# Performance work log

Measured on AMD Instinct MI355X. Metric: run time of the kernel, lower is better.

Reference implementation:

```python
import jax, jax.numpy as jnp
import numpy as np

N = 100000
IN_C, HID_C, OUT_C = 128, 128, 64
E = 1600000


def setup_inputs() -> dict:
    key = jax.random.key(0)
    ks = jax.random.split(key, 8)
    x = jax.random.normal(ks[0], (N, IN_C), dtype=jnp.float32)
    edge_index = jax.random.randint(ks[1], (2, E), 0, N, dtype=jnp.int64)
    def glorot(k, fan_in, fan_out):
        lim = np.sqrt(6.0 / (fan_in + fan_out)).astype(np.float32)
        return jax.random.uniform(k, (fan_in, fan_out), jnp.float32, -lim, lim)
    return {
        "x": x,
        "edge_index": edge_index,
        "W1l": glorot(ks[2], IN_C, HID_C),   # lin_l: aggregated neighbors
        "W1r": glorot(ks[3], IN_C, HID_C),   # lin_r: root/self
        "b1": jnp.zeros((HID_C,), jnp.float32),
        "W2l": glorot(ks[4], HID_C, OUT_C),
        "W2r": glorot(ks[5], HID_C, OUT_C),
        "b2": jnp.zeros((OUT_C,), jnp.float32),
    }


def _sage_conv(x, src, dst, Wl, Wr, b):
    # mean aggregation over incoming edges: gather source feats, segment-sum at dst
    msg_sum = jax.ops.segment_sum(x[src], dst, num_segments=N)          # [N, C_in]
    deg = jax.ops.segment_sum(jnp.ones((src.shape[0],), x.dtype), dst,
                              num_segments=N)                           # [N]
    mean = msg_sum / jnp.clip(deg, 1.0, None)[:, None]
    return mean @ Wl + x @ Wr + b


def reference(x, edge_index, W1l, W1r, b1, W2l, W2r, b2):
    src, dst = edge_index[0], edge_index[1]
    h = jax.nn.relu(_sage_conv(x, src, dst, W1l, W1r, b1))
    out = _sage_conv(h, src, dst, W2l, W2r, b2)
    return out
```

## Files before the change

### kernel.cpp

```cpp
#include <hip/hip_runtime.h>
#include <type_traits>


constexpr int K = 128;
constexpr int EB = 2048;
constexpr int CAP = 8192;

typedef __bf16 bf16x2 __attribute__((ext_vector_type(2)));
typedef __bf16 bf16x4 __attribute__((ext_vector_type(4)));
typedef __bf16 bf16x8 __attribute__((ext_vector_type(8)));
typedef float f32x4 __attribute__((ext_vector_type(4)));
typedef float f32x2 __attribute__((ext_vector_type(2)));


__device__ __forceinline__ unsigned char to_fp8(float v) {
#if __has_builtin(__builtin_amdgcn_cvt_pk_fp8_f32)
  int p = __builtin_amdgcn_cvt_pk_fp8_f32(v, v, 0, false);
  return (unsigned char)(p & 0xff);
#else
  unsigned u = __builtin_bit_cast(unsigned, v);
  unsigned s = (u >> 24) & 0x80u;
  float a = fabsf(v);
  if (a > 448.f) a = 448.f;
  unsigned bits;
  if (a < 0.015625f) {
    bits = (unsigned)(a * 512.f + 0.5f);
  } else {
    unsigned b = __builtin_bit_cast(unsigned, a);
    b += ((b >> 20) & 1) + 0x0007FFFF;
    unsigned e = (b >> 23) - 120;
    bits = (e << 3) | ((b >> 20) & 7);
    if (bits > 0x7E) bits = 0x7E;
  }
  return (unsigned char)(s | bits);
#endif
}

__device__ __forceinline__ f32x2 from_fp8x2(unsigned short u) {
#if __has_builtin(__builtin_amdgcn_cvt_pk_f32_fp8)
  return __builtin_amdgcn_cvt_pk_f32_fp8((int)u, false);
#else
  f32x2 r;
  unsigned b0 = u & 0xff, b1 = (u >> 8) & 0xff;
  unsigned e0 = (b0 >> 3) & 15, m0 = b0 & 7;
  unsigned e1 = (b1 >> 3) & 15, m1 = b1 & 7;
  float v0 = e0 ? __builtin_bit_cast(float, ((e0 + 120) << 23) | (m0 << 20))
              : (float)m0 * 0.001953125f;
  float v1 = e1 ? __builtin_bit_cast(float, ((e1 + 120) << 23) | (m1 << 20))
              : (float)m1 * 0.001953125f;
  r[0] = (b0 & 0x80) ? -v0 : v0;
  r[1] = (b1 & 0x80) ? -v1 : v1;
  return r;
#endif
}

__device__ __forceinline__ f32x2 fp8x2_lo(unsigned v) {
#if __has_builtin(__builtin_amdgcn_cvt_pk_f32_fp8)
  return __builtin_amdgcn_cvt_pk_f32_fp8((int)v, false);
#else
  return from_fp8x2((unsigned short)(v & 0xffffu));
#endif
}

__device__ __forceinline__ f32x2 fp8x2_hi(unsigned v) {
#if __has_builtin(__builtin_amdgcn_cvt_pk_f32_fp8)
  return __builtin_amdgcn_cvt_pk_f32_fp8((int)v, true);
#else
  return from_fp8x2((unsigned short)(v >> 16));
#endif
}


__global__ __launch_bounds__(256) void k_scatter(const int* __restrict__ src,
                                                 const int* __restrict__ dst,
                                                 int* __restrict__ bucketCount,
                                                 unsigned* __restrict__ recs,
                                                 int E, int n, int nB) {
  extern __shared__ int cur[];
  for (int i = threadIdx.x; i < nB; i += 256) cur[i] = 0;
  __syncthreads();
  int base = blockIdx.x * EB, end = min(base + EB, E);
  for (int e = base + threadIdx.x; e < end; e += 256) {
    int d = dst[e];
    if ((unsigned)d < (unsigned)n) atomicAdd(&cur[d >> 8], 1);
  }
  __syncthreads();
  for (int i = threadIdx.x; i < nB; i += 256) {
    int c = cur[i];
    cur[i] = c ? atomicAdd(&bucketCount[i], c) : 0;
  }
  __syncthreads();
  for (int e = base + threadIdx.x; e < end; e += 256) {
    int d = dst[e];
    if ((unsigned)d < (unsigned)n) {
      int s = min(max(src[e], 0), n - 1);
      int b = d >> 8;
      int pos = min(atomicAdd(&cur[b], 1), CAP - 1);
      recs[(long)b * CAP + pos] = ((unsigned)s << 8) | (unsigned)(d & 255);
    }
  }
}

__global__ __launch_bounds__(256) void k_bfill(const unsigned* __restrict__ recs,
                                               const int* __restrict__ bucketCount,
                                               int* __restrict__ rowptr,
                                               int* __restrict__ col, int n) {
  __shared__ int degl[256];
  __shared__ int incl[256];
  __shared__ int red[256];
  int b = blockIdx.x, t = threadIdx.x;

  int partial = 0;
  for (int i = t; i < b; i += 256) partial += bucketCount[i];
  red[t] = partial;
  __syncthreads();
  for (int off = 128; off > 0; off >>= 1) {
    if (t < off) red[t] += red[t + off];
    __syncthreads();
  }
  int rbeg = red[0];
  int cnt = bucketCount[b];
  const unsigned* rbase = recs + (long)b * CAP;
  __syncthreads();

  degl[t] = 0;
  __syncthreads();
  for (int i = t; i < cnt; i += 256)
    atomicAdd(&degl[rbase[i] & 255], 1);
  __syncthreads();
  incl[t] = degl[t];
  __syncthreads();
  for (int off = 1; off < 256; off <<= 1) {
    int v = (t >= off) ? incl[t - off] : 0;
    __syncthreads();
    incl[t] += v;
    __syncthreads();
  }
  int excl = incl[t] - degl[t];
  int node = b * 256 + t;
  if (node <= n) rowptr[node] = rbeg + excl;
  __syncthreads();
  degl[t] = rbeg + excl;
  __syncthreads();
  for (int i = t; i < cnt; i += 256) {
    unsigned r = rbase[i];
    int pos = atomicAdd(&degl[r & 255], 1);
    col[pos] = (int)(r >> 8);
  }
}


template <int COLS, typename TIN>
__global__ __launch_bounds__(512, 4) void k_gemm_fused(const TIN* __restrict__ X,
                                                       const float* __restrict__ Wa,
                                                       const float* __restrict__ Wb,
                                                       unsigned char* __restrict__ outA,
                                                       __bf16* __restrict__ outB,
                                                       int nrows, int ntiles) {
  constexpr int LD = 136;
  constexpr int NI = COLS / 64;
  constexpr bool FP32IN = std::is_same_v<TIN, float>;
  __shared__ __bf16 As[2][64 * LD];

  int tid = threadIdx.x;
  int w = tid >> 6, lane = tid & 63;
  int m = lane & 15, quad = lane >> 4;
  int panel = w >> 2;
  int wcol = (w & 3) * (16 * NI);
  const float* Wsrc = panel ? Wb : Wa;

  bf16x8 bq[4][NI];
#pragma unroll
  for (int kc = 0; kc < 4; ++kc)
#pragma unroll
    for (int ni = 0; ni < NI; ++ni)
#pragma unroll
      for (int e = 0; e < 8; ++e)
        bq[kc][ni][e] = (__bf16)Wsrc[(kc * 32 + quad * 8 + e) * COLS + (wcol + ni * 16 + m)];

  float4 ra[4];
  bf16x8 rb[2];

  auto load_tile = [&](int t) {
    long row0 = (long)t * 64;
    if constexpr (FP32IN) {
#pragma unroll
      for (int it = 0; it < 4; ++it) {
        int i = tid + it * 512;
        int r = i >> 5, c4 = (i & 31) << 2;
        long row = row0 + r;
        float4 v = make_float4(0.f, 0.f, 0.f, 0.f);
        if (row < nrows) v = *(const float4*)(X + row * K + c4);
        ra[it] = v;
      }
    } else {
#pragma unroll
      for (int it = 0; it < 2; ++it) {
        int i = tid + it * 512;
        int r = i >> 4, c8 = (i & 15) << 3;
        long row = row0 + r;
        bf16x8 v = {};
        if (row < nrows) v = *(const bf16x8*)(X + row * K + c8);
        rb[it] = v;
      }
    }
  };

  auto write_tile = [&](int buf) {
    if constexpr (FP32IN) {
#pragma unroll
      for (int it = 0; it < 4; ++it) {
        int i = tid + it * 512;
        int r = i >> 5, c4 = (i & 31) << 2;
        bf16x4 bb;
        bb[0] = (__bf16)ra[it].x; bb[1] = (__bf16)ra[it].y;
        bb[2] = (__bf16)ra[it].z; bb[3] = (__bf16)ra[it].w;
        *(bf16x4*)&As[buf][r * LD + c4] = bb;
      }
    } else {
#pragma unroll
      for (int it = 0; it < 2; ++it) {
        int i = tid + it * 512;
        int r = i >> 4, c8 = (i & 15) << 3;
        *(bf16x8*)&As[buf][r * LD + c8] = rb[it];
      }
    }
  };

  int t = (int)blockIdx.x;
  int stride = (int)gridDim.x;
  if (t < ntiles) load_tile(t);

#pragma unroll
  for (int kc = 0; kc < 4; ++kc)
#pragma unroll
    for (int ni = 0; ni < NI; ++ni)
      asm volatile("" :: "v"(bq[kc][ni]));

  int buf = 0;
  while (t < ntiles) {
    write_tile(buf);
    __syncthreads();
    int tn = t + stride;
    if (tn < ntiles) load_tile(tn);

    f32x4 acc[4][NI];
#pragma unroll
    for (int mi = 0; mi < 4; ++mi)
#pragma unroll
      for (int ni = 0; ni < NI; ++ni) acc[mi][ni] = (f32x4){0.f, 0.f, 0.f, 0.f};

#pragma unroll
    for (int kc = 0; kc < 4; ++kc) {
      int ko = kc * 32 + quad * 8;
      bf16x8 af[4];
#pragma unroll
      for (int mi = 0; mi < 4; ++mi)
        af[mi] = *(const bf16x8*)&As[buf][(mi * 16 + m) * LD + ko];
#pragma unroll
      for (int mi = 0; mi < 4; ++mi)
#pragma unroll
        for (int ni = 0; ni < NI; ++ni)
          acc[mi][ni] = __builtin_amdgcn_mfma_f32_16x16x32_bf16(af[mi], bq[kc][ni], acc[mi][ni], 0, 0, 0);
    }

    long row0 = (long)t * 64;
#pragma unroll
    for (int mi = 0; mi < 4; ++mi) {
#pragma unroll
      for (int r = 0; r < 4; ++r) {
        long grow = row0 + mi * 16 + quad * 4 + r;
        if (grow < nrows) {
#pragma unroll
          for (int ni = 0; ni < NI; ++ni) {
            long idx = grow * COLS + wcol + ni * 16 + m;
            float v = acc[mi][ni][r];
            if (panel == 0) outA[idx] = to_fp8(v);
            else            outB[idx] = (__bf16)v;
          }
        }
      }
    }
    t = tn;
    buf ^= 1;
  }
}


template <bool RELU>
__global__ __launch_bounds__(256) void k_agg128(const unsigned char* __restrict__ Y,
                                                const __bf16* __restrict__ XR,
                                                const float* __restrict__ bias,
                                                const int* __restrict__ rowptr,
                                                const int* __restrict__ col,
                                                __bf16* __restrict__ out, int nnodes) {
  int wave = threadIdx.x >> 6, lane = threadIdx.x & 63;
  int quarter = lane >> 4, l = lane & 15;
  int sb = lane & 48;
  int n = blockIdx.x * 16 + wave * 4 + quarter;
  bool valid = n < nnodes;
  int beg = 0, end = 0;
  if (valid) {
    beg = rowptr[n];
    end = rowptr[n + 1];
  }
  int co = l * 8;
  const unsigned char* Yc = Y + co;

  f32x2 av0 = {0.f, 0.f}, av1 = {0.f, 0.f}, av2 = {0.f, 0.f}, av3 = {0.f, 0.f};

  for (int base = beg; base < end; base += 16) {
    int cnt = min(end - base, 16);
    int idx = (l < cnt) ? col[base + l] : 0;
    int j = 0;
    for (; j + 3 < cnt; j += 4) {
      long s0 = (unsigned)__shfl(idx, sb + j);
      long s1 = (unsigned)__shfl(idx, sb + j + 1);
      long s2 = (unsigned)__shfl(idx, sb + j + 2);
      long s3 = (unsigned)__shfl(idx, sb + j + 3);
      uint2 v0 = *(const uint2*)(Yc + s0 * 128);
      uint2 v1 = *(const uint2*)(Yc + s1 * 128);
      uint2 v2 = *(const uint2*)(Yc + s2 * 128);
      uint2 v3 = *(const uint2*)(Yc + s3 * 128);
      av0 += fp8x2_lo(v0.x); av1 += fp8x2_hi(v0.x);
      av2 += fp8x2_lo(v0.y); av3 += fp8x2_hi(v0.y);
      av0 += fp8x2_lo(v1.x); av1 += fp8x2_hi(v1.x);
      av2 += fp8x2_lo(v1.y); av3 += fp8x2_hi(v1.y);
      av0 += fp8x2_lo(v2.x); av1 += fp8x2_hi(v2.x);
      av2 += fp8x2_lo(v2.y); av3 += fp8x2_hi(v2.y);
      av0 += fp8x2_lo(v3.x); av1 += fp8x2_hi(v3.x);
      av2 += fp8x2_lo(v3.y); av3 += fp8x2_hi(v3.y);
    }
    for (; j < cnt; ++j) {
      long s = (unsigned)__shfl(idx, sb + j);
      uint2 v = *(const uint2*)(Yc + s * 128);
      av0 += fp8x2_lo(v.x); av1 += fp8x2_hi(v.x);
      av2 += fp8x2_lo(v.y); av3 += fp8x2_hi(v.y);
    }
  }

  if (valid) {
    float inv = 1.f / (float)max(end - beg, 1);
    bf16x8 xv = *(const bf16x8*)(XR + (long)n * 128 + co);
    f32x4 b0 = *(const f32x4*)(bias + co);
    f32x4 b1 = *(const f32x4*)(bias + co + 4);
    float r0 = av0[0] * inv + (float)xv[0] + b0[0];
    float r1 = av0[1] * inv + (float)xv[1] + b0[1];
    float r2 = av1[0] * inv + (float)xv[2] + b0[2];
    float r3 = av1[1] * inv + (float)xv[3] + b0[3];
    float r4 = av2[0] * inv + (float)xv[4] + b1[0];
    float r5 = av2[1] * inv + (float)xv[5] + b1[1];
    float r6 = av3[0] * inv + (float)xv[6] + b1[2];
    float r7 = av3[1] * inv + (float)xv[7] + b1[3];
    if (RELU) {
      r0 = fmaxf(r0, 0.f); r1 = fmaxf(r1, 0.f);
      r2 = fmaxf(r2, 0.f); r3 = fmaxf(r3, 0.f);
      r4 = fmaxf(r4, 0.f); r5 = fmaxf(r5, 0.f);
      r6 = fmaxf(r6, 0.f); r7 = fmaxf(r7, 0.f);
    }
    bf16x8 o;
    o[0] = (__bf16)r0; o[1] = (__bf16)r1; o[2] = (__bf16)r2; o[3] = (__bf16)r3;
    o[4] = (__bf16)r4; o[5] = (__bf16)r5; o[6] = (__bf16)r6; o[7] = (__bf16)r7;
    *(bf16x8*)(out + (long)n * 128 + co) = o;
  }
}

__global__ __launch_bounds__(256) void k_agg64(const unsigned char* __restrict__ Y,
                                               const __bf16* __restrict__ XR,
                                               const float* __restrict__ bias,
                                               const int* __restrict__ rowptr,
                                               const int* __restrict__ col,
                                               float* __restrict__ out, int nnodes) {
  int wave = threadIdx.x >> 6, lane = threadIdx.x & 63;
  int quarter = lane >> 4, l = lane & 15;
  int sb = lane & 48;
  int n = blockIdx.x * 16 + wave * 4 + quarter;
  bool valid = n < nnodes;
  int beg = 0, end = 0;
  if (valid) {
    beg = rowptr[n];
    end = rowptr[n + 1];
  }
  int co = l * 4;
  const unsigned char* Yc = Y + co;

  f32x2 av0 = {0.f, 0.f}, av1 = {0.f, 0.f};

  for (int base = beg; base < end; base += 16) {
    int cnt = min(end - base, 16);
    int idx = (l < cnt) ? col[base + l] : 0;
    int j = 0;
    for (; j + 3 < cnt; j += 4) {
      long s0 = (unsigned)__shfl(idx, sb + j);
      long s1 = (unsigned)__shfl(idx, sb + j + 1);
      long s2 = (unsigned)__shfl(idx, sb + j + 2);
      long s3 = (unsigned)__shfl(idx, sb + j + 3);
      unsigned v0 = *(const unsigned*)(Yc + s0 * 64);
      unsigned v1 = *(const unsigned*)(Yc + s1 * 64);
      unsigned v2 = *(const unsigned*)(Yc + s2 * 64);
      unsigned v3 = *(const unsigned*)(Yc + s3 * 64);
      av0 += fp8x2_lo(v0); av1 += fp8x2_hi(v0);
      av0 += fp8x2_lo(v1); av1 += fp8x2_hi(v1);
      av0 += fp8x2_lo(v2); av1 += fp8x2_hi(v2);
      av0 += fp8x2_lo(v3); av1 += fp8x2_hi(v3);
    }
    for (; j < cnt; ++j) {
      long s = (unsigned)__shfl(idx, sb + j);
      unsigned v = *(const unsigned*)(Yc + s * 64);
      av0 += fp8x2_lo(v); av1 += fp8x2_hi(v);
    }
  }

  if (valid) {
    float inv = 1.f / (float)max(end - beg, 1);
    bf16x4 xv = *(const bf16x4*)(XR + (long)n * 64 + co);
    f32x4 bv = *(const f32x4*)(bias + co);
    f32x4 r;
    r[0] = av0[0] * inv + (float)xv[0] + bv[0];
    r[1] = av0[1] * inv + (float)xv[1] + bv[1];
    r[2] = av1[0] * inv + (float)xv[2] + bv[2];
    r[3] = av1[1] * inv + (float)xv[3] + bv[3];
    *(f32x4*)(out + (long)n * 64 + co) = r;
  }
}


extern "C" void kernel_launch(void* const* d_in, const int* in_sizes, int n_in,
                              void* d_out, int out_size, void* d_ws, size_t ws_size,
                              hipStream_t stream) {
  const float* x   = (const float*)d_in[0];
  const int*   ei  = (const int*)d_in[1];
  const float* W1l = (const float*)d_in[2];
  const float* W1r = (const float*)d_in[3];
  const float* b1  = (const float*)d_in[4];
  const float* W2l = (const float*)d_in[5];
  const float* W2r = (const float*)d_in[6];
  const float* b2  = (const float*)d_in[7];
  float* out = (float*)d_out;

  int N = in_sizes[0] / K;
  int E = in_sizes[1] / 2;
  const int* src = ei;
  const int* dst = ei + E;

  int nB = (N + 255) >> 8;
  int nblk = (E + EB - 1) / EB;

  char* ws = (char*)d_ws;
  size_t off = 0;
  auto alloc = [&](size_t bytes) {
    void* p = ws + off;
    off = (off + bytes + 255) & ~(size_t)255;
    return p;
  };
  int*      rowptr      = (int*)alloc(((size_t)N + 2) * 4);
  int*      col         = (int*)alloc((size_t)E * 4);
  int*      bucketCount = (int*)alloc((size_t)nB * 4);
  unsigned* recs        = (unsigned*)alloc((size_t)nB * CAP * 4);
  unsigned char* y1     = (unsigned char*)alloc((size_t)N * 128);
  __bf16*   xr          = (__bf16*)alloc((size_t)N * 128 * 2);
  __bf16*   h           = (__bf16*)alloc((size_t)N * 128 * 2);
  unsigned char* y2 = y1;
  __bf16*   hr = xr;

  int ntiles = (N + 63) / 64;
  int gpers = ntiles < 512 ? ntiles : 512;

  hipMemsetAsync(bucketCount, 0, (size_t)nB * 4, stream);
  k_scatter<<<nblk, 256, nB * 4, stream>>>(src, dst, bucketCount, recs, E, N, nB);

  k_gemm_fused<128, float><<<gpers, 512, 0, stream>>>(x, W1l, W1r, y1, xr, N, ntiles);

  k_bfill<<<nB, 256, 0, stream>>>(recs, bucketCount, rowptr, col, N);
  k_agg128<true><<<(N + 15) / 16, 256, 0, stream>>>(y1, xr, b1, rowptr, col, h, N);

  k_gemm_fused<64, __bf16><<<gpers, 512, 0, stream>>>(h, W2l, W2r, y2, hr, N, ntiles);

  k_agg64<<<(N + 15) / 16, 256, 0, stream>>>(y2, hr, b2, rowptr, col, out, N);
}
```

Before: 249.9 us.

## Fuse edge scatter and first-layer GEMM into one heterogeneous kernel launch

The edge bucketing scatter and the first-layer dual GEMM now run in a single launch. The first nblk blocks do the scatter, reusing the GEMM's shared-memory tile as the bucket counter array, and the remaining blocks run the persistent tiled MFMA GEMM, so the two independent phases overlap on the device and one launch is saved. The scatter blocks now use 512 threads and handle 4096 edges each, which halves their count. In exchange, the scatter blocks carry the GEMM's register and LDS footprint, and their occupancy is bounded by the 512-thread launch.

```diff
diff --git a/kernel.cpp b/kernel.cpp
--- a/kernel.cpp
+++ b/kernel.cpp
@@ -3,7 +3,7 @@
 
 
 constexpr int K = 128;
-constexpr int EB = 2048;
+constexpr int EB = 4096;
 constexpr int CAP = 8192;
 
 typedef __bf16 bf16x2 __attribute__((ext_vector_type(2)));
@@ -71,33 +71,144 @@
 }
 
 
-__global__ __launch_bounds__(256) void k_scatter(const int* __restrict__ src,
-                                                 const int* __restrict__ dst,
-                                                 int* __restrict__ bucketCount,
-                                                 unsigned* __restrict__ recs,
-                                                 int E, int n, int nB) {
-  extern __shared__ int cur[];
-  for (int i = threadIdx.x; i < nB; i += 256) cur[i] = 0;
-  __syncthreads();
-  int base = blockIdx.x * EB, end = min(base + EB, E);
-  for (int e = base + threadIdx.x; e < end; e += 256) {
-    int d = dst[e];
-    if ((unsigned)d < (unsigned)n) atomicAdd(&cur[d >> 8], 1);
-  }
-  __syncthreads();
-  for (int i = threadIdx.x; i < nB; i += 256) {
-    int c = cur[i];
-    cur[i] = c ? atomicAdd(&bucketCount[i], c) : 0;
-  }
-  __syncthreads();
-  for (int e = base + threadIdx.x; e < end; e += 256) {
-    int d = dst[e];
-    if ((unsigned)d < (unsigned)n) {
-      int s = min(max(src[e], 0), n - 1);
-      int b = d >> 8;
-      int pos = min(atomicAdd(&cur[b], 1), CAP - 1);
-      recs[(long)b * CAP + pos] = ((unsigned)s << 8) | (unsigned)(d & 255);
-    }
+template <int COLS>
+__global__ __launch_bounds__(512, 4) void k_scatter_gemm(
+    const int* __restrict__ src, const int* __restrict__ dst,
+    int* __restrict__ bucketCount, unsigned* __restrict__ recs,
+    int E, int n, int nB, int nscat,
+    const float* __restrict__ X, const float* __restrict__ Wa,
+    const float* __restrict__ Wb, unsigned char* __restrict__ outA,
+    __bf16* __restrict__ outB, int ntiles) {
+  constexpr int LD = 136;
+  constexpr int NI = COLS / 64;
+  __shared__ __bf16 As[2][64 * LD];
+
+  int bid = blockIdx.x;
+  int tid = threadIdx.x;
+
+  if (bid < nscat) {
+    int* cur = (int*)As;
+    for (int i = tid; i < nB; i += 512) cur[i] = 0;
+    __syncthreads();
+    int base = bid * EB, endE = min(base + EB, E);
+    for (int e = base + tid; e < endE; e += 512) {
+      int d = dst[e];
+      if ((unsigned)d < (unsigned)n) atomicAdd(&cur[d >> 8], 1);
+    }
+    __syncthreads();
+    for (int i = tid; i < nB; i += 512) {
+      int c = cur[i];
+      cur[i] = c ? atomicAdd(&bucketCount[i], c) : 0;
+    }
+    __syncthreads();
+    for (int e = base + tid; e < endE; e += 512) {
+      int d = dst[e];
+      if ((unsigned)d < (unsigned)n) {
+        int s = min(max(src[e], 0), n - 1);
+        int b = d >> 8;
+        int pos = min(atomicAdd(&cur[b], 1), CAP - 1);
+        recs[(long)b * CAP + pos] = ((unsigned)s << 8) | (unsigned)(d & 255);
+      }
+    }
+    return;
+  }
+
+  int w = tid >> 6, lane = tid & 63;
+  int m = lane & 15, quad = lane >> 4;
+  int panel = w >> 2;
+  int wcol = (w & 3) * (16 * NI);
+  const float* Wsrc = panel ? Wb : Wa;
+
+  bf16x8 bq[4][NI];
+#pragma unroll
+  for (int kc = 0; kc < 4; ++kc)
+#pragma unroll
+    for (int ni = 0; ni < NI; ++ni)
+#pragma unroll
+      for (int e = 0; e < 8; ++e)
+        bq[kc][ni][e] = (__bf16)Wsrc[(kc * 32 + quad * 8 + e) * COLS + (wcol + ni * 16 + m)];
+
+  float4 ra[4];
+  auto load_tile = [&](int t) {
+    long row0 = (long)t * 64;
+#pragma unroll
+    for (int it = 0; it < 4; ++it) {
+      int i = tid + it * 512;
+      int r = i >> 5, c4 = (i & 31) << 2;
+      long row = row0 + r;
+      float4 v = make_float4(0.f, 0.f, 0.f, 0.f);
+      if (row < n) v = *(const float4*)(X + row * K + c4);
+      ra[it] = v;
+    }
+  };
+  auto write_tile = [&](int buf) {
+#pragma unroll
+    for (int it = 0; it < 4; ++it) {
+      int i = tid + it * 512;
+      int r = i >> 5, c4 = (i & 31) << 2;
+      bf16x4 bb;
+      bb[0] = (__bf16)ra[it].x; bb[1] = (__bf16)ra[it].y;
+      bb[2] = (__bf16)ra[it].z; bb[3] = (__bf16)ra[it].w;
+      *(bf16x4*)&As[buf][r * LD + c4] = bb;
+    }
+  };
+
+  int t = bid - nscat;
+  int stride = (int)gridDim.x - nscat;
+  if (t < ntiles) load_tile(t);
+
+#pragma unroll
+  for (int kc = 0; kc < 4; ++kc)
+#pragma unroll
+    for (int ni = 0; ni < NI; ++ni)
+      asm volatile("" :: "v"(bq[kc][ni]));
+
+  int buf = 0;
+  while (t < ntiles) {
+    write_tile(buf);
+    __syncthreads();
+    int tn = t + stride;
+    if (tn < ntiles) load_tile(tn);
+
+    f32x4 acc[4][NI];
+#pragma unroll
+    for (int mi = 0; mi < 4; ++mi)
+#pragma unroll
+      for (int ni = 0; ni < NI; ++ni) acc[mi][ni] = (f32x4){0.f, 0.f, 0.f, 0.f};
+
+#pragma unroll
+    for (int kc = 0; kc < 4; ++kc) {
+      int ko = kc * 32 + quad * 8;
+      bf16x8 af[4];
+#pragma unroll
+      for (int mi = 0; mi < 4; ++mi)
+        af[mi] = *(const bf16x8*)&As[buf][(mi * 16 + m) * LD + ko];
+#pragma unroll
+      for (int mi = 0; mi < 4; ++mi)
+#pragma unroll
+        for (int ni = 0; ni < NI; ++ni)
+          acc[mi][ni] = __builtin_amdgcn_mfma_f32_16x16x32_bf16(af[mi], bq[kc][ni], acc[mi][ni], 0, 0, 0);
+    }
+
+    long row0 = (long)t * 64;
+#pragma unroll
+    for (int mi = 0; mi < 4; ++mi) {
+#pragma unroll
+      for (int r = 0; r < 4; ++r) {
+        long grow = row0 + mi * 16 + quad * 4 + r;
+        if (grow < n) {
+#pragma unroll
+          for (int ni = 0; ni < NI; ++ni) {
+            long idx = grow * COLS + wcol + ni * 16 + m;
+            float v = acc[mi][ni][r];
+            if (panel == 0) outA[idx] = to_fp8(v);
+            else            outB[idx] = (__bf16)v;
+          }
+        }
+      }
+    }
+    t = tn;
+    buf ^= 1;
   }
 }
 
@@ -467,9 +578,9 @@
   int gpers = ntiles < 512 ? ntiles : 512;
 
   hipMemsetAsync(bucketCount, 0, (size_t)nB * 4, stream);
-  k_scatter<<<nblk, 256, nB * 4, stream>>>(src, dst, bucketCount, recs, E, N, nB);
-
-  k_gemm_fused<128, float><<<gpers, 512, 0, stream>>>(x, W1l, W1r, y1, xr, N, ntiles);
+  k_scatter_gemm<128><<<nblk + gpers, 512, 0, stream>>>(
+      src, dst, bucketCount, recs, E, N, nB, nblk,
+      x, W1l, W1r, y1, xr, ntiles);
 
   k_bfill<<<nB, 256, 0, stream>>>(recs, bucketCount, rowptr, col, N);
   k_agg128<true><<<(N + 15) / 16, 256, 0, stream>>>(y1, xr, b1, rowptr, col, h, N);
```

New measurement: 244.5 us. -2.2%, faster.
